# Kernel optimization log

Hardware: AMD Instinct MI355X
Metric: run time of the kernel (lower is better)

The kernel has to match this reference:

```python
import jax, jax.numpy as jnp
import numpy as np

N, E, F, H, C, B = 50000, 1_600_000, 128, 128, 10, 512


def setup_inputs() -> dict:
    key = jax.random.key(0)
    ks = jax.random.split(key, 12)
    inp = {
        "x": jax.random.normal(ks[0], (N, F), dtype=jnp.float32),
        "edge_index": jax.random.randint(ks[1], (2, E), 0, N, dtype=jnp.int32),
        "batch": jnp.sort(jax.random.randint(ks[2], (N,), 0, B, dtype=jnp.int32)),
        "edge_weight": jax.random.uniform(ks[3], (E,), dtype=jnp.float32),
        "W1": jax.random.normal(ks[4], (F, H), dtype=jnp.float32) * 0.05,
        "b1": jnp.zeros((H,), dtype=jnp.float32),
        "W2": jax.random.normal(ks[5], (H, H), dtype=jnp.float32) * 0.05,
        "b2": jnp.zeros((H,), dtype=jnp.float32),
        "W3": jax.random.normal(ks[6], (H, H), dtype=jnp.float32) * 0.05,
        "b3": jnp.zeros((H,), dtype=jnp.float32),
        "Wlin": jax.random.normal(ks[7], (H, C), dtype=jnp.float32) * 0.05,
        "blin": jnp.zeros((C,), dtype=jnp.float32),
    }
    return inp


def reference(x, edge_index, batch, edge_weight, W1, b1, W2, b2, W3, b3, Wlin, blin):
    n = x.shape[0]
    src, dst = edge_index[0], edge_index[1]
    loops = jnp.arange(n, dtype=src.dtype)
    src_f = jnp.concatenate([src, loops])  # edges + self-loops
    dst_f = jnp.concatenate([dst, loops])

    def make_norm(fill_value):
        # GCN symmetric normalization: D^-1/2 (A + fill*I) D^-1/2 on edge weights
        ew = jnp.concatenate([edge_weight, jnp.full((n,), fill_value, dtype=edge_weight.dtype)])
        deg = jax.ops.segment_sum(ew, dst_f, num_segments=n)
        dinv = jnp.where(deg > 0, deg ** -0.5, 0.0)
        return dinv[src_f] * ew * dinv[dst_f]

    # conv1 was built as GCNConv(in, hidden, out_channels) -> third positional arg is
    # `improved`, truthy => self-loop fill value 2.0; conv2/3 use 1.0.
    norm1 = make_norm(2.0)
    norm = make_norm(1.0)

    def gcn_conv(h, W, b, nrm):
        h = h @ W                                   # [N, H]
        msg = h[src_f] * nrm[:, None]               # [E+N, H] gather
        return jax.ops.segment_sum(msg, dst_f, num_segments=n) + b

    h = jax.nn.relu(gcn_conv(x, W1, b1, norm1))
    h = jax.nn.relu(gcn_conv(h, W2, b2, norm))
    h = gcn_conv(h, W3, b3, norm)

    # global_mean_pool over graph ids
    sums = jax.ops.segment_sum(h, batch, num_segments=B)
    cnt = jax.ops.segment_sum(jnp.ones((n,), dtype=h.dtype), batch, num_segments=B)
    pooled = sums / jnp.maximum(cnt, 1.0)[:, None]

    # dropout is identity in eval mode
    return pooled @ Wlin + blin
```

## Files before the change

kernel.cpp:

```cpp
#include <hip/hip_runtime.h>
#include <hip/hip_fp16.h>

#define F 128
#define HID 128
#define NCLS 10
#define CAP 80
#define NBIN 256
#define NPB 196
#define SCAP 7168
#define EPT 8
#define HLS 136

typedef short short8 __attribute__((ext_vector_type(8)));
typedef float float4v __attribute__((ext_vector_type(4)));
typedef float float2v __attribute__((ext_vector_type(2)));

__device__ __forceinline__ unsigned short f2bf(float f) {
    unsigned int u = __float_as_uint(f);
    unsigned int r = (u + 0x7FFFu + ((u >> 16) & 1u)) >> 16;
    return (unsigned short)r;
}
__device__ __forceinline__ float bf2f(unsigned int h) {
    return __uint_as_float(h << 16);
}
__device__ __forceinline__ unsigned char f2fp8(float a) {
    return (unsigned char)(__builtin_amdgcn_cvt_pk_fp8_f32(a, 0.f, 0, false) & 0xFF);
}

__global__ __launch_bounds__(256) void bin_prep_kernel(
    const int* __restrict__ ei, const float* __restrict__ ew,
    int* __restrict__ gcur, uint2* __restrict__ staging, int E, int nbb,
    const float* __restrict__ W1, const float* __restrict__ W2,
    const float* __restrict__ W3, const float* __restrict__ Wlin,
    const float* __restrict__ blin, const float* __restrict__ b3,
    unsigned short* __restrict__ Wp, unsigned short* __restrict__ Wp3s,
    float* __restrict__ bL) {
    __shared__ int lhist[NBIN];
    __shared__ int lscan[NBIN];
    __shared__ int lbase[NBIN];
    __shared__ uint2 lent[256 * EPT];
    int tid = threadIdx.x;

    if ((int)blockIdx.x < nbb) {
        lhist[tid] = 0;
        __syncthreads();

        unsigned int rpk[EPT];
        unsigned short rd[EPT];
        unsigned short rloc[EPT];
        int base = blockIdx.x * (256 * EPT);
#pragma unroll
        for (int i = 0; i < EPT; i++) {
            int e = base + tid + i * 256;
            if (e < E) {
                int s = ei[e];
                int d = ei[E + e];
                unsigned int q = (unsigned int)(ew[e] * 65535.0f + 0.5f);
                rpk[i] = (q << 16) | (unsigned int)s;
                rd[i] = (unsigned short)d;
                rloc[i] = (unsigned short)atomicAdd(&lhist[d / NPB], 1);
            } else {
                rpk[i] = 0u; rd[i] = 0; rloc[i] = 0xFFFF;
            }
        }
        __syncthreads();

        lscan[tid] = lhist[tid];
        __syncthreads();
        for (int off = 1; off < NBIN; off <<= 1) {
            int t = (tid >= off) ? lscan[tid - off] : 0;
            __syncthreads();
            lscan[tid] += t;
            __syncthreads();
        }
        lbase[tid] = atomicAdd(&gcur[tid], lhist[tid]);
        __syncthreads();

#pragma unroll
        for (int i = 0; i < EPT; i++) {
            if (rloc[i] != 0xFFFF) {
                int bin = (int)rd[i] / NPB;
                int slot = (lscan[bin] - lhist[bin]) + (int)rloc[i];
                lent[slot] = make_uint2(rpk[i], (unsigned int)rd[i]);
            }
        }
        __syncthreads();

        int total = lscan[NBIN - 1];
        for (int j = tid; j < total; j += 256) {
            uint2 t = lent[j];
            int bin = (int)t.y / NPB;
            int pos = lbase[bin] + (j - (lscan[bin] - lhist[bin]));
            if (pos < SCAP) staging[(size_t)bin * SCAP + pos] = t;
        }
    } else {
        int b = blockIdx.x - nbb;
        if (b < 128) {
            int widx = b >> 6;
            const float* W = (widx == 0) ? W1 : W2;
            int idx = (b & 63) * 256 + tid;
            int j = idx & 7;
            int l = (idx >> 3) & 63;
            int nt = (idx >> 9) & 7;
            int kt = idx >> 12;
            int k = kt * 32 + ((l >> 4) << 3) + j;
            int n = nt * 16 + (l & 15);
            Wp[widx * 16384 + idx] = f2bf(W[k * HID + n]);
        } else if (b < 136) {
            int idx = (b - 128) * 256 + tid;
            int j = idx & 7;
            int l = (idx >> 3) & 63;
            int kt = idx >> 9;
            int k = kt * 32 + ((l >> 4) << 3) + j;
            int n = l & 15;
            float v = 0.f;
            if (n < NCLS) {
                for (int m = 0; m < HID; m++)
                    v += W3[k * HID + m] * Wlin[m * NCLS + n];
            }
            Wp3s[idx] = f2bf(v);
        } else {
            if (tid < NCLS) {
                float bl = blin[tid];
                for (int j = 0; j < HID; j++) bl += b3[j] * Wlin[j * NCLS + tid];
                bL[tid] = bl;
            }
        }
    }
}

__global__ __launch_bounds__(1024, 8) void build_gemm1_kernel(
    const uint2* __restrict__ staging, const int* __restrict__ gcur,
    unsigned int* __restrict__ colw, int* __restrict__ cnt,
    float* __restrict__ dinv1, float* __restrict__ dinv0, int N, int nbins,
    const float* __restrict__ X, const unsigned short* __restrict__ Wp,
    unsigned char* __restrict__ Yb8) {
    __shared__ unsigned int lbuck[NPB * CAP];
    __shared__ int lcnt[NPB];
    int tid = threadIdx.x;

    if ((int)blockIdx.x < nbins) {
        int bin = blockIdx.x;
        int node0 = bin * NPB;

        for (int n = tid; n < NPB; n += 1024) lcnt[n] = 0;
        __syncthreads();

        int bcnt = gcur[bin];
        if (bcnt > SCAP) bcnt = SCAP;
        const uint2* st = staging + (size_t)bin * SCAP;
        for (int i = tid; i < bcnt; i += 1024) {
            uint2 t = st[i];
            int dl = (int)t.y - node0;
            int pos = atomicAdd(&lcnt[dl], 1);
            if (pos < CAP) lbuck[dl * CAP + pos] = t.x;
        }
        __syncthreads();

        for (int it = 0; it < NPB; it += 128) {
            int nl = it + (tid >> 3);
            int lane = tid & 7;
            if (nl < NPB) {
                int gn = node0 + nl;
                if (gn < N) {
                    int c = lcnt[nl];
                    if (c > CAP) c = CAP;
                    float s = 0.f;
                    for (int j = lane; j < c; j += 8)
                        s += (float)(lbuck[nl * CAP + j] >> 16);
                    s += __shfl_down(s, 4, 8);
                    s += __shfl_down(s, 2, 8);
                    s += __shfl_down(s, 1, 8);
                    if (lane == 0) {
                        float deg = s * (1.0f / 65535.0f);
                        cnt[gn] = c;
                        dinv1[gn] = 1.0f / sqrtf(deg + 2.0f);
                        dinv0[gn] = 1.0f / sqrtf(deg + 1.0f);
                    }
                }
            }
        }
        __syncthreads();

        int nvalid = N - node0;
        if (nvalid > NPB) nvalid = NPB;
        if (nvalid <= 0) return;
        int nslots = nvalid * (CAP / 4);
        uint4* dst4 = (uint4*)(colw + (size_t)node0 * CAP);
        const uint4* src4 = (const uint4*)lbuck;
        for (int i = tid; i < nslots; i += 1024) {
            int rowi = i / (CAP / 4);
            int slot = i - rowi * (CAP / 4);
            int c = lcnt[rowi];
            if (c > CAP) c = CAP;
            if (slot * 4 < c) dst4[i] = src4[i];
        }
    } else {
        int tile = blockIdx.x - nbins;
        int wave = tid >> 6, lane = tid & 63;
        int quad = lane >> 4, m = lane & 15;
        int row0 = tile * 256 + wave * 16;
        if (row0 >= N) return;
        int row = row0 + m;
        int rowc = row < N ? row : N - 1;

        short8 a[4];
        const float4* xrow = (const float4*)(X + (size_t)rowc * F);
#pragma unroll
        for (int kt = 0; kt < 4; kt++) {
            float4 p0 = xrow[kt * 8 + quad * 2];
            float4 p1 = xrow[kt * 8 + quad * 2 + 1];
            short8 v;
            v[0] = (short)f2bf(p0.x); v[1] = (short)f2bf(p0.y);
            v[2] = (short)f2bf(p0.z); v[3] = (short)f2bf(p0.w);
            v[4] = (short)f2bf(p1.x); v[5] = (short)f2bf(p1.y);
            v[6] = (short)f2bf(p1.z); v[7] = (short)f2bf(p1.w);
            a[kt] = v;
        }

#pragma unroll
        for (int nt = 0; nt < 8; nt++) {
            float4v c = {0.f, 0.f, 0.f, 0.f};
#pragma unroll
            for (int kt = 0; kt < 4; kt++) {
                short8 b = *(const short8*)(Wp + (((kt * 8 + nt) * 64 + lane) << 3));
                c = __builtin_amdgcn_mfma_f32_16x16x32_bf16(a[kt], b, c, 0, 0, 0);
            }
#pragma unroll
            for (int r = 0; r < 4; r++) {
                int gr = row0 + quad * 4 + r;
                if (gr < N) Yb8[(size_t)gr * HID + nt * 16 + m] = f2fp8(c[r]);
            }
        }
    }
}

__device__ __forceinline__ void agg_acc8(float f, const uint4& h,
                                         float2v acc[8]) {
    float2v fv = {f, f};
    acc[0] += fv * __builtin_amdgcn_cvt_pk_f32_fp8(h.x, false);
    acc[1] += fv * __builtin_amdgcn_cvt_pk_f32_fp8(h.x, true);
    acc[2] += fv * __builtin_amdgcn_cvt_pk_f32_fp8(h.y, false);
    acc[3] += fv * __builtin_amdgcn_cvt_pk_f32_fp8(h.y, true);
    acc[4] += fv * __builtin_amdgcn_cvt_pk_f32_fp8(h.z, false);
    acc[5] += fv * __builtin_amdgcn_cvt_pk_f32_fp8(h.z, true);
    acc[6] += fv * __builtin_amdgcn_cvt_pk_f32_fp8(h.w, false);
    acc[7] += fv * __builtin_amdgcn_cvt_pk_f32_fp8(h.w, true);
}

__device__ __forceinline__ void agg_b4(const unsigned int w[8], int t0, int fl,
                                       const uint4* __restrict__ hin4,
                                       const float* __restrict__ dinv,
                                       float2v acc[8]) {
    uint4 h[4];
    float dv[4];
#pragma unroll
    for (int t = 0; t < 4; t++) h[t] = hin4[(w[t0 + t] & 0xFFFFu) * 8 + fl];
#pragma unroll
    for (int t = 0; t < 4; t++) dv[t] = dinv[w[t0 + t] & 0xFFFFu];
#pragma unroll
    for (int t = 0; t < 4; t++) {
        float f = (float)(w[t0 + t] >> 16) * (1.0f / 65535.0f) * dv[t];
        agg_acc8(f, h[t], acc);
    }
}

__device__ __forceinline__ void agg_p32(unsigned int pk, int q, int fl,
                                        const uint4* __restrict__ hin4,
                                        const float* __restrict__ dinv,
                                        float2v acc[8]) {
    unsigned int w[8];
#pragma unroll
    for (int t = 0; t < 4; t++) {
        w[2 * t]     = (unsigned int)__shfl((int)pk, t * 8 + 2 * q, 32);
        w[2 * t + 1] = (unsigned int)__shfl((int)pk, t * 8 + 2 * q + 1, 32);
    }
    agg_b4(w, 0, fl, hin4, dinv, acc);
    agg_b4(w, 4, fl, hin4, dinv, acc);
}

__device__ __forceinline__ void agg_p8(unsigned int pk, int j0, int q, int fl,
                                       const uint4* __restrict__ hin4,
                                       const float* __restrict__ dinv,
                                       float2v acc[8]) {
    unsigned int w0 = (unsigned int)__shfl((int)pk, j0 + 2 * q, 32);
    unsigned int w1 = (unsigned int)__shfl((int)pk, j0 + 2 * q + 1, 32);
    uint4 h0 = hin4[(w0 & 0xFFFFu) * 8 + fl];
    uint4 h1 = hin4[(w1 & 0xFFFFu) * 8 + fl];
    float d0 = dinv[w0 & 0xFFFFu];
    float d1 = dinv[w1 & 0xFFFFu];
    agg_acc8((float)(w0 >> 16) * (1.0f / 65535.0f) * d0, h0, acc);
    agg_acc8((float)(w1 >> 16) * (1.0f / 65535.0f) * d1, h1, acc);
}

__device__ __forceinline__ void agg_node_fp8(int g, int lane,
                                             const unsigned char* __restrict__ hin,
                                             const unsigned int* __restrict__ colw,
                                             const int* __restrict__ cnt,
                                             const float* __restrict__ dinv,
                                             float fill,
                                             const float* __restrict__ bias,
                                             unsigned short* __restrict__ hl_row) {
    float dv = dinv[g];
    int c = cnt[g];
    if (c > CAP) c = CAP;
    const unsigned int* row = colw + (size_t)g * CAP;
    const uint4* hin4 = (const uint4*)hin;

    unsigned int pk[3];
#pragma unroll
    for (int k = 0; k < 3; k++) {
        int idx = lane + k * 32;
        pk[k] = (idx < c) ? row[idx] : 0u;
    }

    int q = lane >> 3;
    int fl = lane & 7;

    float2v acc[8];
#pragma unroll
    for (int i = 0; i < 8; i++) acc[i] = (float2v){0.f, 0.f};

    agg_p32(pk[0], q, fl, hin4, dinv, acc);
    if (c > 32) {
        int cc = c - 32;
        if (cc > 32) cc = 32;
        for (int j = 0; j < cc; j += 8) agg_p8(pk[1], j, q, fl, hin4, dinv, acc);
    }
    if (c > 64) {
        int cc = c - 64;
        for (int j = 0; j < cc; j += 8) agg_p8(pk[2], j, q, fl, hin4, dinv, acc);
    }

#pragma unroll
    for (int i = 0; i < 8; i++) {
        acc[i][0] += __shfl_down(acc[i][0], 16, 32);
        acc[i][1] += __shfl_down(acc[i][1], 16, 32);
        acc[i][0] += __shfl_down(acc[i][0], 8, 32);
        acc[i][1] += __shfl_down(acc[i][1], 8, 32);
    }

    if (q == 0) {
        uint4 hv = hin4[(size_t)g * 8 + fl];
        float2v ws = {fill * dv, fill * dv};
        float2v dvv = {dv, dv};
        acc[0] = (acc[0] + ws * __builtin_amdgcn_cvt_pk_f32_fp8(hv.x, false)) * dvv;
        acc[1] = (acc[1] + ws * __builtin_amdgcn_cvt_pk_f32_fp8(hv.x, true)) * dvv;
        acc[2] = (acc[2] + ws * __builtin_amdgcn_cvt_pk_f32_fp8(hv.y, false)) * dvv;
        acc[3] = (acc[3] + ws * __builtin_amdgcn_cvt_pk_f32_fp8(hv.y, true)) * dvv;
        acc[4] = (acc[4] + ws * __builtin_amdgcn_cvt_pk_f32_fp8(hv.z, false)) * dvv;
        acc[5] = (acc[5] + ws * __builtin_amdgcn_cvt_pk_f32_fp8(hv.z, true)) * dvv;
        acc[6] = (acc[6] + ws * __builtin_amdgcn_cvt_pk_f32_fp8(hv.w, false)) * dvv;
        acc[7] = (acc[7] + ws * __builtin_amdgcn_cvt_pk_f32_fp8(hv.w, true)) * dvv;

        const float2v* b2 = (const float2v*)(bias + fl * 16);
        uint4 o0, o1;
        unsigned int ow[8];
#pragma unroll
        for (int i = 0; i < 8; i++) {
            float2v v = acc[i] + b2[i];
            float v0 = fmaxf(v[0], 0.f);
            float v1 = fmaxf(v[1], 0.f);
            ow[i] = (unsigned int)f2bf(v0) | ((unsigned int)f2bf(v1) << 16);
        }
        o0 = make_uint4(ow[0], ow[1], ow[2], ow[3]);
        o1 = make_uint4(ow[4], ow[5], ow[6], ow[7]);
        *(uint4*)(hl_row + fl * 16) = o0;
        *(uint4*)(hl_row + fl * 16 + 8) = o1;
    }
}

__global__ __launch_bounds__(512) void agg_gemm128_kernel(const unsigned char* __restrict__ hin,
                                                          const unsigned int* __restrict__ colw,
                                                          const int* __restrict__ cnt,
                                                          const float* __restrict__ dinv,
                                                          const float* __restrict__ bias,
                                                          const unsigned short* __restrict__ Wp2,
                                                          unsigned char* __restrict__ Yb8,
                                                          int N) {
    __shared__ unsigned short hl[16 * HLS];
    __shared__ unsigned char Ol8[16 * 128];

    int tid = threadIdx.x;
    int gl = tid >> 5, lane = tid & 31;
    int row0 = blockIdx.x * 16;
    int g = row0 + gl;

    if (g < N) {
        agg_node_fp8(g, lane, hin, colw, cnt, dinv, 2.0f, bias, hl + gl * HLS);
    } else if ((lane >> 3) == 0) {
        *(uint4*)(hl + gl * HLS + (lane & 7) * 16) = make_uint4(0u, 0u, 0u, 0u);
        *(uint4*)(hl + gl * HLS + (lane & 7) * 16 + 8) = make_uint4(0u, 0u, 0u, 0u);
    }
    __syncthreads();

    int nt = tid >> 6;
    int lane64 = tid & 63;
    int quad = lane64 >> 4, m = lane64 & 15;

    short8 a[4];
#pragma unroll
    for (int kt = 0; kt < 4; kt++)
        a[kt] = *(const short8*)(hl + m * HLS + kt * 32 + quad * 8);

    float4v c = {0.f, 0.f, 0.f, 0.f};
#pragma unroll
    for (int kt = 0; kt < 4; kt++) {
        short8 b = *(const short8*)(Wp2 + (((kt * 8 + nt) * 64 + lane64) << 3));
        c = __builtin_amdgcn_mfma_f32_16x16x32_bf16(a[kt], b, c, 0, 0, 0);
    }
#pragma unroll
    for (int r = 0; r < 4; r++)
        Ol8[(quad * 4 + r) * 128 + nt * 16 + m] = f2fp8(c[r]);
    __syncthreads();

    if (tid < 128) {
        int gr = row0 + (tid >> 3);
        if (gr < N)
            ((uint4*)(Yb8 + (size_t)gr * 128))[tid & 7] = ((const uint4*)Ol8)[tid];
    }
}

__global__ __launch_bounds__(512) void agg_gemm16_kernel(const unsigned char* __restrict__ hin,
                                                         const unsigned int* __restrict__ colw,
                                                         const int* __restrict__ cnt,
                                                         const float* __restrict__ dinv,
                                                         const float* __restrict__ bias,
                                                         const unsigned short* __restrict__ Wp3s,
                                                         unsigned short* __restrict__ g3s,
                                                         int N) {
    __shared__ unsigned short hl[16 * HLS];

    int tid = threadIdx.x;
    int gl = tid >> 5, lane = tid & 31;
    int row0 = blockIdx.x * 16;
    int g = row0 + gl;

    if (g < N) {
        agg_node_fp8(g, lane, hin, colw, cnt, dinv, 1.0f, bias, hl + gl * HLS);
    } else if ((lane >> 3) == 0) {
        *(uint4*)(hl + gl * HLS + (lane & 7) * 16) = make_uint4(0u, 0u, 0u, 0u);
        *(uint4*)(hl + gl * HLS + (lane & 7) * 16 + 8) = make_uint4(0u, 0u, 0u, 0u);
    }
    __syncthreads();

    if (tid < 64) {
        int lane64 = tid;
        int quad = lane64 >> 4, m = lane64 & 15;
        short8 a[4];
#pragma unroll
        for (int kt = 0; kt < 4; kt++)
            a[kt] = *(const short8*)(hl + m * HLS + kt * 32 + quad * 8);
        float4v c = {0.f, 0.f, 0.f, 0.f};
#pragma unroll
        for (int kt = 0; kt < 4; kt++) {
            short8 b = *(const short8*)(Wp3s + ((kt * 64 + lane64) << 3));
            c = __builtin_amdgcn_mfma_f32_16x16x32_bf16(a[kt], b, c, 0, 0, 0);
        }
#pragma unroll
        for (int r = 0; r < 4; r++) {
            int gr = row0 + quad * 4 + r;
            if (gr < N) g3s[(size_t)gr * 16 + m] = f2bf(c[r]);
        }
    }
}

__device__ __forceinline__ void agg3_slot(unsigned int pk, int lane2off,
                                          const unsigned short* __restrict__ g3s,
                                          const float* __restrict__ dinv,
                                          float& ax, float& ay) {
    unsigned int w[8];
    unsigned int h[8];
    float dvv[8];
#pragma unroll
    for (int t = 0; t < 8; t++)
        w[t] = (unsigned int)__shfl((int)pk, t, 8);
#pragma unroll
    for (int t = 0; t < 8; t++)
        h[t] = *(const unsigned int*)(g3s + (w[t] & 0xFFFFu) * 16 + lane2off);
#pragma unroll
    for (int t = 0; t < 8; t++)
        dvv[t] = dinv[w[t] & 0xFFFFu];
#pragma unroll
    for (int t = 0; t < 8; t++) {
        float f = (float)(w[t] >> 16) * (1.0f / 65535.0f) * dvv[t];
        ax += f * bf2f(h[t] & 0xFFFFu);
        ay += f * bf2f(h[t] >> 16);
    }
}

__global__ __launch_bounds__(256) void agg3_kernel(const unsigned short* __restrict__ g3s,
                                                   const unsigned int* __restrict__ colw,
                                                   const int* __restrict__ cnt,
                                                   const float* __restrict__ dinv,
                                                   unsigned short* __restrict__ h3s, int N) {
    int g = (blockIdx.x * blockDim.x + threadIdx.x) >> 3;
    int lane = threadIdx.x & 7;
    if (g >= N) return;

    float dv = dinv[g];
    int c = cnt[g];
    if (c > CAP) c = CAP;
    const unsigned int* row = colw + (size_t)g * CAP;
    int lane2off = lane * 2;

    unsigned int pk[10];
#pragma unroll
    for (int k = 0; k < 10; k++) {
        int idx = lane + k * 8;
        pk[k] = (idx < c) ? row[idx] : 0u;
    }

    float ax = 0.f, ay = 0.f;
#pragma unroll
    for (int slot = 0; slot < 10; slot++) {
        int base = slot * 8;
        if (c > base) agg3_slot(pk[slot], lane2off, g3s, dinv, ax, ay);
    }

    unsigned int hv = *(const unsigned int*)(g3s + (size_t)g * 16 + lane2off);
    ax = (ax + dv * bf2f(hv & 0xFFFFu)) * dv;
    ay = (ay + dv * bf2f(hv >> 16)) * dv;

    unsigned int o = (unsigned int)f2bf(ax) | ((unsigned int)f2bf(ay) << 16);
    *(unsigned int*)(h3s + (size_t)g * 16 + lane2off) = o;
}

__global__ __launch_bounds__(256) void pool3_kernel(const unsigned short* __restrict__ h3s,
                                                    const int* __restrict__ batch,
                                                    const float* __restrict__ bL,
                                                    const float* __restrict__ blin,
                                                    float* __restrict__ out, int N, int B) {
    int wave = (blockIdx.x * blockDim.x + threadIdx.x) >> 6;
    int lane = threadIdx.x & 63;
    if (wave >= B) return;
    int g = wave;
    int d = lane & 15, sub = lane >> 4;

    int lo = 0, hi = N;
    while (lo < hi) { int m = (lo + hi) >> 1; if (batch[m] < g) lo = m + 1; else hi = m; }
    int s0 = lo;
    hi = N;
    while (lo < hi) { int m = (lo + hi) >> 1; if (batch[m] < g + 1) lo = m + 1; else hi = m; }
    int s1 = lo;

    float p = 0.f;
    for (int v = s0 + sub; v < s1; v += 4)
        p += bf2f((unsigned int)h3s[(size_t)v * 16 + d]);
    p += __shfl_down(p, 32, 64);
    p += __shfl_down(p, 16, 64);

    if (lane < NCLS) {
        int cntv = s1 - s0;
        float r = (cntv > 0) ? (p / (float)cntv + bL[d]) : blin[d];
        out[g * NCLS + d] = r;
    }
}

extern "C" void kernel_launch(void* const* d_in, const int* in_sizes, int n_in,
                              void* d_out, int out_size, void* d_ws, size_t ws_size,
                              hipStream_t stream) {
    const float* x    = (const float*)d_in[0];
    const int*   ei   = (const int*)d_in[1];
    const int*   batch= (const int*)d_in[2];
    const float* ew   = (const float*)d_in[3];
    const float* W1   = (const float*)d_in[4];
    const float* b1   = (const float*)d_in[5];
    const float* W2   = (const float*)d_in[6];
    const float* b2   = (const float*)d_in[7];
    const float* W3   = (const float*)d_in[8];
    const float* b3   = (const float*)d_in[9];
    const float* Wlin = (const float*)d_in[10];
    const float* blin = (const float*)d_in[11];
    float* out = (float*)d_out;

    int N = in_sizes[0] / F;
    int E = in_sizes[1] / 2;
    int B = out_size / NCLS;

    char* p = (char*)d_ws;
    auto alloc = [&](size_t bytes) -> void* {
        void* r = (void*)p;
        p += (bytes + 255) & ~(size_t)255;
        return r;
    };
    int*            cnt   = (int*)alloc((size_t)N * 4);
    float*          dinv1 = (float*)alloc((size_t)N * 4);
    float*          dinv0 = (float*)alloc((size_t)N * 4);
    int*            gcur  = (int*)alloc(NBIN * 4);
    float*          bL    = (float*)alloc(16 * 4);
    unsigned int*   colw  = (unsigned int*)alloc((size_t)N * CAP * 4);
    unsigned short* Wp    = (unsigned short*)alloc(2 * 16384 * 2);
    unsigned short* Wp3s  = (unsigned short*)alloc(2048 * 2);
    unsigned char*  bufA  = (unsigned char*)alloc((size_t)N * HID);
    unsigned char*  bufB  = (unsigned char*)alloc((size_t)N * HID);
    unsigned short* g3s   = (unsigned short*)alloc((size_t)N * 16 * 2);
    unsigned short* h3s   = (unsigned short*)alloc((size_t)N * 16 * 2);
    uint2*          staging = (uint2*)alloc((size_t)NBIN * SCAP * 8);

    int tb = 256;
    int nbins = (N + NPB - 1) / NPB;
    int nbb = (E + tb * EPT - 1) / (tb * EPT);
    int g1tiles = (N + 255) / 256;

    hipMemsetAsync(gcur, 0, NBIN * 4, stream);
    bin_prep_kernel<<<nbb + 137, tb, 0, stream>>>(ei, ew, gcur, staging, E, nbb,
                                                  W1, W2, W3, Wlin, blin, b3,
                                                  Wp, Wp3s, bL);
    build_gemm1_kernel<<<nbins + g1tiles, 1024, 0, stream>>>(staging, gcur, colw, cnt,
                                                             dinv1, dinv0, N, nbins,
                                                             x, Wp, bufA);

    int fused_blocks = (N + 15) / 16;
    int agg3_blocks = ((N * 8) + tb - 1) / tb;

    agg_gemm128_kernel<<<fused_blocks, 512, 0, stream>>>(bufA, colw, cnt, dinv1, b1,
                                                         Wp + 16384, bufB, N);
    agg_gemm16_kernel<<<fused_blocks, 512, 0, stream>>>(bufB, colw, cnt, dinv0, b2,
                                                        Wp3s, g3s, N);
    agg3_kernel<<<agg3_blocks, tb, 0, stream>>>(g3s, colw, cnt, dinv0, h3s, N);
    pool3_kernel<<<((B * 64) + tb - 1) / tb, tb, 0, stream>>>(h3s, batch, bL, blin,
                                                              out, N, B);
}
```

Baseline: 231.9 us.

## Fuse tail aggregation layers and pooling into one cooperative persistent kernel

Replaces the four tail launches (layer-2 agg+GEMM, layer-3 agg+GEMM, final aggregation, mean pool) with one cooperative kernel that loops over tiles and separates the phases with grid-wide syncs. It also folds the source-side dinv factor into the stored features (scaling GEMM outputs by dinv0), so the later gathers skip the per-edge dinv loads. This removes launch gaps and tail drain between the kernels. In exchange it adds grid barriers, caps the grid at 1024 persistent blocks with forced occupancy of 8 blocks of 512 threads, and changes fp8/bf16 rounding because values are pre-scaled before quantization.

```diff
diff --git a/kernel.cpp b/kernel.cpp
--- a/kernel.cpp
+++ b/kernel.cpp
@@ -1,5 +1,8 @@
 #include <hip/hip_runtime.h>
 #include <hip/hip_fp16.h>
+#include <hip/hip_cooperative_groups.h>
+
+namespace cg = cooperative_groups;
 
 #define F 128
 #define HID 128
@@ -248,6 +251,7 @@
     acc[7] += fv * __builtin_amdgcn_cvt_pk_f32_fp8(h.w, true);
 }
 
+template <bool GD>
 __device__ __forceinline__ void agg_b4(const unsigned int w[8], int t0, int fl,
                                        const uint4* __restrict__ hin4,
                                        const float* __restrict__ dinv,
@@ -256,15 +260,19 @@
     float dv[4];
 #pragma unroll
     for (int t = 0; t < 4; t++) h[t] = hin4[(w[t0 + t] & 0xFFFFu) * 8 + fl];
-#pragma unroll
-    for (int t = 0; t < 4; t++) dv[t] = dinv[w[t0 + t] & 0xFFFFu];
+    if (GD) {
+#pragma unroll
+        for (int t = 0; t < 4; t++) dv[t] = dinv[w[t0 + t] & 0xFFFFu];
+    }
 #pragma unroll
     for (int t = 0; t < 4; t++) {
-        float f = (float)(w[t0 + t] >> 16) * (1.0f / 65535.0f) * dv[t];
+        float f = (float)(w[t0 + t] >> 16) * (1.0f / 65535.0f);
+        if (GD) f *= dv[t];
         agg_acc8(f, h[t], acc);
     }
 }
 
+template <bool GD>
 __device__ __forceinline__ void agg_p32(unsigned int pk, int q, int fl,
                                         const uint4* __restrict__ hin4,
                                         const float* __restrict__ dinv,
@@ -275,10 +283,11 @@
         w[2 * t]     = (unsigned int)__shfl((int)pk, t * 8 + 2 * q, 32);
         w[2 * t + 1] = (unsigned int)__shfl((int)pk, t * 8 + 2 * q + 1, 32);
     }
-    agg_b4(w, 0, fl, hin4, dinv, acc);
-    agg_b4(w, 4, fl, hin4, dinv, acc);
-}
-
+    agg_b4<GD>(w, 0, fl, hin4, dinv, acc);
+    agg_b4<GD>(w, 4, fl, hin4, dinv, acc);
+}
+
+template <bool GD>
 __device__ __forceinline__ void agg_p8(unsigned int pk, int j0, int q, int fl,
                                        const uint4* __restrict__ hin4,
                                        const float* __restrict__ dinv,
@@ -287,12 +296,14 @@
     unsigned int w1 = (unsigned int)__shfl((int)pk, j0 + 2 * q + 1, 32);
     uint4 h0 = hin4[(w0 & 0xFFFFu) * 8 + fl];
     uint4 h1 = hin4[(w1 & 0xFFFFu) * 8 + fl];
-    float d0 = dinv[w0 & 0xFFFFu];
-    float d1 = dinv[w1 & 0xFFFFu];
-    agg_acc8((float)(w0 >> 16) * (1.0f / 65535.0f) * d0, h0, acc);
-    agg_acc8((float)(w1 >> 16) * (1.0f / 65535.0f) * d1, h1, acc);
-}
-
+    float f0 = (float)(w0 >> 16) * (1.0f / 65535.0f);
+    float f1 = (float)(w1 >> 16) * (1.0f / 65535.0f);
+    if (GD) { f0 *= dinv[w0 & 0xFFFFu]; f1 *= dinv[w1 & 0xFFFFu]; }
+    agg_acc8(f0, h0, acc);
+    agg_acc8(f1, h1, acc);
+}
+
+template <bool GD>
 __device__ __forceinline__ void agg_node_fp8(int g, int lane,
                                              const unsigned char* __restrict__ hin,
                                              const unsigned int* __restrict__ colw,
@@ -321,15 +332,15 @@
 #pragma unroll
     for (int i = 0; i < 8; i++) acc[i] = (float2v){0.f, 0.f};
 
-    agg_p32(pk[0], q, fl, hin4, dinv, acc);
+    agg_p32<GD>(pk[0], q, fl, hin4, dinv, acc);
     if (c > 32) {
         int cc = c - 32;
         if (cc > 32) cc = 32;
-        for (int j = 0; j < cc; j += 8) agg_p8(pk[1], j, q, fl, hin4, dinv, acc);
+        for (int j = 0; j < cc; j += 8) agg_p8<GD>(pk[1], j, q, fl, hin4, dinv, acc);
     }
     if (c > 64) {
         int cc = c - 64;
-        for (int j = 0; j < cc; j += 8) agg_p8(pk[2], j, q, fl, hin4, dinv, acc);
+        for (int j = 0; j < cc; j += 8) agg_p8<GD>(pk[2], j, q, fl, hin4, dinv, acc);
     }
 
 #pragma unroll
@@ -342,7 +353,8 @@
 
     if (q == 0) {
         uint4 hv = hin4[(size_t)g * 8 + fl];
-        float2v ws = {fill * dv, fill * dv};
+        float wsv = GD ? fill * dv : fill;
+        float2v ws = {wsv, wsv};
         float2v dvv = {dv, dv};
         acc[0] = (acc[0] + ws * __builtin_amdgcn_cvt_pk_f32_fp8(hv.x, false)) * dvv;
         acc[1] = (acc[1] + ws * __builtin_amdgcn_cvt_pk_f32_fp8(hv.x, true)) * dvv;
@@ -370,190 +382,175 @@
     }
 }
 
-__global__ __launch_bounds__(512) void agg_gemm128_kernel(const unsigned char* __restrict__ hin,
-                                                          const unsigned int* __restrict__ colw,
-                                                          const int* __restrict__ cnt,
-                                                          const float* __restrict__ dinv,
-                                                          const float* __restrict__ bias,
-                                                          const unsigned short* __restrict__ Wp2,
-                                                          unsigned char* __restrict__ Yb8,
-                                                          int N) {
+__global__ __launch_bounds__(512, 8) void fused_tail_kernel(
+    const unsigned char* __restrict__ bufA,
+    const unsigned int* __restrict__ colw, const int* __restrict__ cnt,
+    const float* __restrict__ dinv1, const float* __restrict__ dinv0,
+    const float* __restrict__ b1, const float* __restrict__ b2,
+    const unsigned short* __restrict__ Wp2,
+    const unsigned short* __restrict__ Wp3s,
+    unsigned char* __restrict__ bufB, unsigned short* __restrict__ g3s,
+    unsigned short* __restrict__ h3s,
+    const int* __restrict__ batch, const float* __restrict__ bL,
+    const float* __restrict__ blin, float* __restrict__ out,
+    int N, int B) {
+    cg::grid_group grid = cg::this_grid();
     __shared__ unsigned short hl[16 * HLS];
     __shared__ unsigned char Ol8[16 * 128];
 
     int tid = threadIdx.x;
     int gl = tid >> 5, lane = tid & 31;
-    int row0 = blockIdx.x * 16;
-    int g = row0 + gl;
-
-    if (g < N) {
-        agg_node_fp8(g, lane, hin, colw, cnt, dinv, 2.0f, bias, hl + gl * HLS);
-    } else if ((lane >> 3) == 0) {
-        *(uint4*)(hl + gl * HLS + (lane & 7) * 16) = make_uint4(0u, 0u, 0u, 0u);
-        *(uint4*)(hl + gl * HLS + (lane & 7) * 16 + 8) = make_uint4(0u, 0u, 0u, 0u);
-    }
-    __syncthreads();
-
-    int nt = tid >> 6;
-    int lane64 = tid & 63;
-    int quad = lane64 >> 4, m = lane64 & 15;
-
-    short8 a[4];
-#pragma unroll
-    for (int kt = 0; kt < 4; kt++)
-        a[kt] = *(const short8*)(hl + m * HLS + kt * 32 + quad * 8);
-
-    float4v c = {0.f, 0.f, 0.f, 0.f};
-#pragma unroll
-    for (int kt = 0; kt < 4; kt++) {
-        short8 b = *(const short8*)(Wp2 + (((kt * 8 + nt) * 64 + lane64) << 3));
-        c = __builtin_amdgcn_mfma_f32_16x16x32_bf16(a[kt], b, c, 0, 0, 0);
-    }
-#pragma unroll
-    for (int r = 0; r < 4; r++)
-        Ol8[(quad * 4 + r) * 128 + nt * 16 + m] = f2fp8(c[r]);
-    __syncthreads();
-
-    if (tid < 128) {
-        int gr = row0 + (tid >> 3);
-        if (gr < N)
-            ((uint4*)(Yb8 + (size_t)gr * 128))[tid & 7] = ((const uint4*)Ol8)[tid];
-    }
-}
-
-__global__ __launch_bounds__(512) void agg_gemm16_kernel(const unsigned char* __restrict__ hin,
-                                                         const unsigned int* __restrict__ colw,
-                                                         const int* __restrict__ cnt,
-                                                         const float* __restrict__ dinv,
-                                                         const float* __restrict__ bias,
-                                                         const unsigned short* __restrict__ Wp3s,
-                                                         unsigned short* __restrict__ g3s,
-                                                         int N) {
-    __shared__ unsigned short hl[16 * HLS];
-
-    int tid = threadIdx.x;
-    int gl = tid >> 5, lane = tid & 31;
-    int row0 = blockIdx.x * 16;
-    int g = row0 + gl;
-
-    if (g < N) {
-        agg_node_fp8(g, lane, hin, colw, cnt, dinv, 1.0f, bias, hl + gl * HLS);
-    } else if ((lane >> 3) == 0) {
-        *(uint4*)(hl + gl * HLS + (lane & 7) * 16) = make_uint4(0u, 0u, 0u, 0u);
-        *(uint4*)(hl + gl * HLS + (lane & 7) * 16 + 8) = make_uint4(0u, 0u, 0u, 0u);
-    }
-    __syncthreads();
-
-    if (tid < 64) {
-        int lane64 = tid;
+    int ntiles = (N + 15) >> 4;
+
+    for (int t = blockIdx.x; t < ntiles; t += gridDim.x) {
+        int row0 = t * 16;
+        int g = row0 + gl;
+        if (g < N) {
+            agg_node_fp8<true>(g, lane, bufA, colw, cnt, dinv1, 2.0f, b1,
+                               hl + gl * HLS);
+        } else if ((lane >> 3) == 0) {
+            *(uint4*)(hl + gl * HLS + (lane & 7) * 16) = make_uint4(0u, 0u, 0u, 0u);
+            *(uint4*)(hl + gl * HLS + (lane & 7) * 16 + 8) = make_uint4(0u, 0u, 0u, 0u);
+        }
+        __syncthreads();
+
+        int nt = tid >> 6;
+        int lane64 = tid & 63;
         int quad = lane64 >> 4, m = lane64 & 15;
+
         short8 a[4];
 #pragma unroll
         for (int kt = 0; kt < 4; kt++)
             a[kt] = *(const short8*)(hl + m * HLS + kt * 32 + quad * 8);
+
         float4v c = {0.f, 0.f, 0.f, 0.f};
 #pragma unroll
         for (int kt = 0; kt < 4; kt++) {
-            short8 b = *(const short8*)(Wp3s + ((kt * 64 + lane64) << 3));
+            short8 b = *(const short8*)(Wp2 + (((kt * 8 + nt) * 64 + lane64) << 3));
             c = __builtin_amdgcn_mfma_f32_16x16x32_bf16(a[kt], b, c, 0, 0, 0);
         }
 #pragma unroll
         for (int r = 0; r < 4; r++) {
             int gr = row0 + quad * 4 + r;
-            if (gr < N) g3s[(size_t)gr * 16 + m] = f2bf(c[r]);
-        }
-    }
-}
-
-__device__ __forceinline__ void agg3_slot(unsigned int pk, int lane2off,
-                                          const unsigned short* __restrict__ g3s,
-                                          const float* __restrict__ dinv,
-                                          float& ax, float& ay) {
-    unsigned int w[8];
-    unsigned int h[8];
-    float dvv[8];
-#pragma unroll
-    for (int t = 0; t < 8; t++)
-        w[t] = (unsigned int)__shfl((int)pk, t, 8);
-#pragma unroll
-    for (int t = 0; t < 8; t++)
-        h[t] = *(const unsigned int*)(g3s + (w[t] & 0xFFFFu) * 16 + lane2off);
-#pragma unroll
-    for (int t = 0; t < 8; t++)
-        dvv[t] = dinv[w[t] & 0xFFFFu];
-#pragma unroll
-    for (int t = 0; t < 8; t++) {
-        float f = (float)(w[t] >> 16) * (1.0f / 65535.0f) * dvv[t];
-        ax += f * bf2f(h[t] & 0xFFFFu);
-        ay += f * bf2f(h[t] >> 16);
-    }
-}
-
-__global__ __launch_bounds__(256) void agg3_kernel(const unsigned short* __restrict__ g3s,
-                                                   const unsigned int* __restrict__ colw,
-                                                   const int* __restrict__ cnt,
-                                                   const float* __restrict__ dinv,
-                                                   unsigned short* __restrict__ h3s, int N) {
-    int g = (blockIdx.x * blockDim.x + threadIdx.x) >> 3;
-    int lane = threadIdx.x & 7;
-    if (g >= N) return;
-
-    float dv = dinv[g];
-    int c = cnt[g];
-    if (c > CAP) c = CAP;
-    const unsigned int* row = colw + (size_t)g * CAP;
-    int lane2off = lane * 2;
-
-    unsigned int pk[10];
-#pragma unroll
-    for (int k = 0; k < 10; k++) {
-        int idx = lane + k * 8;
-        pk[k] = (idx < c) ? row[idx] : 0u;
-    }
-
-    float ax = 0.f, ay = 0.f;
-#pragma unroll
-    for (int slot = 0; slot < 10; slot++) {
-        int base = slot * 8;
-        if (c > base) agg3_slot(pk[slot], lane2off, g3s, dinv, ax, ay);
-    }
-
-    unsigned int hv = *(const unsigned int*)(g3s + (size_t)g * 16 + lane2off);
-    ax = (ax + dv * bf2f(hv & 0xFFFFu)) * dv;
-    ay = (ay + dv * bf2f(hv >> 16)) * dv;
-
-    unsigned int o = (unsigned int)f2bf(ax) | ((unsigned int)f2bf(ay) << 16);
-    *(unsigned int*)(h3s + (size_t)g * 16 + lane2off) = o;
-}
-
-__global__ __launch_bounds__(256) void pool3_kernel(const unsigned short* __restrict__ h3s,
-                                                    const int* __restrict__ batch,
-                                                    const float* __restrict__ bL,
-                                                    const float* __restrict__ blin,
-                                                    float* __restrict__ out, int N, int B) {
-    int wave = (blockIdx.x * blockDim.x + threadIdx.x) >> 6;
-    int lane = threadIdx.x & 63;
-    if (wave >= B) return;
-    int g = wave;
-    int d = lane & 15, sub = lane >> 4;
-
-    int lo = 0, hi = N;
-    while (lo < hi) { int m = (lo + hi) >> 1; if (batch[m] < g) lo = m + 1; else hi = m; }
-    int s0 = lo;
-    hi = N;
-    while (lo < hi) { int m = (lo + hi) >> 1; if (batch[m] < g + 1) lo = m + 1; else hi = m; }
-    int s1 = lo;
-
-    float p = 0.f;
-    for (int v = s0 + sub; v < s1; v += 4)
-        p += bf2f((unsigned int)h3s[(size_t)v * 16 + d]);
-    p += __shfl_down(p, 32, 64);
-    p += __shfl_down(p, 16, 64);
-
-    if (lane < NCLS) {
-        int cntv = s1 - s0;
-        float r = (cntv > 0) ? (p / (float)cntv + bL[d]) : blin[d];
-        out[g * NCLS + d] = r;
+            float sc = (gr < N) ? dinv0[gr] : 0.f;
+            Ol8[(quad * 4 + r) * 128 + nt * 16 + m] = f2fp8(c[r] * sc);
+        }
+        __syncthreads();
+
+        if (tid < 128) {
+            int gr = row0 + (tid >> 3);
+            if (gr < N)
+                ((uint4*)(bufB + (size_t)gr * 128))[tid & 7] = ((const uint4*)Ol8)[tid];
+        }
+    }
+    grid.sync();
+
+    for (int t = blockIdx.x; t < ntiles; t += gridDim.x) {
+        int row0 = t * 16;
+        int g = row0 + gl;
+        if (g < N) {
+            agg_node_fp8<false>(g, lane, bufB, colw, cnt, dinv0, 1.0f, b2,
+                                hl + gl * HLS);
+        } else if ((lane >> 3) == 0) {
+            *(uint4*)(hl + gl * HLS + (lane & 7) * 16) = make_uint4(0u, 0u, 0u, 0u);
+            *(uint4*)(hl + gl * HLS + (lane & 7) * 16 + 8) = make_uint4(0u, 0u, 0u, 0u);
+        }
+        __syncthreads();
+
+        if (tid < 64) {
+            int lane64 = tid;
+            int quad = lane64 >> 4, m = lane64 & 15;
+            short8 a[4];
+#pragma unroll
+            for (int kt = 0; kt < 4; kt++)
+                a[kt] = *(const short8*)(hl + m * HLS + kt * 32 + quad * 8);
+            float4v c = {0.f, 0.f, 0.f, 0.f};
+#pragma unroll
+            for (int kt = 0; kt < 4; kt++) {
+                short8 b = *(const short8*)(Wp3s + ((kt * 64 + lane64) << 3));
+                c = __builtin_amdgcn_mfma_f32_16x16x32_bf16(a[kt], b, c, 0, 0, 0);
+            }
+#pragma unroll
+            for (int r = 0; r < 4; r++) {
+                int gr = row0 + quad * 4 + r;
+                if (gr < N)
+                    g3s[(size_t)gr * 16 + m] = f2bf(c[r] * dinv0[gr]);
+            }
+        }
+        __syncthreads();
+    }
+    grid.sync();
+
+    {
+        int lane8 = tid & 7;
+        int lane2off = lane8 * 2;
+        for (int g = blockIdx.x * 64 + (tid >> 3); g < N; g += gridDim.x * 64) {
+            float dv = dinv0[g];
+            int c = cnt[g];
+            if (c > CAP) c = CAP;
+            const unsigned int* row = colw + (size_t)g * CAP;
+
+            unsigned int pk[10];
+#pragma unroll
+            for (int k = 0; k < 10; k++) {
+                int idx = lane8 + k * 8;
+                pk[k] = (idx < c) ? row[idx] : 0u;
+            }
+
+            float ax = 0.f, ay = 0.f;
+#pragma unroll
+            for (int slot = 0; slot < 10; slot++) {
+                if (c > slot * 8) {
+                    unsigned int w[8];
+                    unsigned int h[8];
+#pragma unroll
+                    for (int tt = 0; tt < 8; tt++)
+                        w[tt] = (unsigned int)__shfl((int)pk[slot], tt, 8);
+#pragma unroll
+                    for (int tt = 0; tt < 8; tt++)
+                        h[tt] = *(const unsigned int*)(g3s + (w[tt] & 0xFFFFu) * 16 + lane2off);
+#pragma unroll
+                    for (int tt = 0; tt < 8; tt++) {
+                        float f = (float)(w[tt] >> 16) * (1.0f / 65535.0f);
+                        ax += f * bf2f(h[tt] & 0xFFFFu);
+                        ay += f * bf2f(h[tt] >> 16);
+                    }
+                }
+            }
+
+            unsigned int hv = *(const unsigned int*)(g3s + (size_t)g * 16 + lane2off);
+            ax = (ax + bf2f(hv & 0xFFFFu)) * dv;
+            ay = (ay + bf2f(hv >> 16)) * dv;
+
+            unsigned int o = (unsigned int)f2bf(ax) | ((unsigned int)f2bf(ay) << 16);
+            *(unsigned int*)(h3s + (size_t)g * 16 + lane2off) = o;
+        }
+    }
+    grid.sync();
+
+    {
+        int lane64 = tid & 63;
+        int d = lane64 & 15, sub = lane64 >> 4;
+        for (int g = blockIdx.x * 8 + (tid >> 6); g < B; g += gridDim.x * 8) {
+            int lo = 0, hi = N;
+            while (lo < hi) { int m = (lo + hi) >> 1; if (batch[m] < g) lo = m + 1; else hi = m; }
+            int s0 = lo;
+            hi = N;
+            while (lo < hi) { int m = (lo + hi) >> 1; if (batch[m] < g + 1) lo = m + 1; else hi = m; }
+            int s1 = lo;
+
+            float p = 0.f;
+            for (int v = s0 + sub; v < s1; v += 4)
+                p += bf2f((unsigned int)h3s[(size_t)v * 16 + d]);
+            p += __shfl_down(p, 32, 64);
+            p += __shfl_down(p, 16, 64);
+
+            if (lane64 < NCLS) {
+                int cntv = s1 - s0;
+                float r = (cntv > 0) ? (p / (float)cntv + bL[d]) : blin[d];
+                out[g * NCLS + d] = r;
+            }
+        }
     }
 }
 
@@ -611,14 +608,24 @@
                                                              dinv1, dinv0, N, nbins,
                                                              x, Wp, bufA);
 
-    int fused_blocks = (N + 15) / 16;
-    int agg3_blocks = ((N * 8) + tb - 1) / tb;
-
-    agg_gemm128_kernel<<<fused_blocks, 512, 0, stream>>>(bufA, colw, cnt, dinv1, b1,
-                                                         Wp + 16384, bufB, N);
-    agg_gemm16_kernel<<<fused_blocks, 512, 0, stream>>>(bufB, colw, cnt, dinv0, b2,
-                                                        Wp3s, g3s, N);
-    agg3_kernel<<<agg3_blocks, tb, 0, stream>>>(g3s, colw, cnt, dinv0, h3s, N);
-    pool3_kernel<<<((B * 64) + tb - 1) / tb, tb, 0, stream>>>(h3s, batch, bL, blin,
-                                                              out, N, B);
-}
+    static int coop_grid = -1;
+    if (coop_grid < 0) {
+        int maxb = 0, ncu = 0;
+        hipOccupancyMaxActiveBlocksPerMultiprocessor(&maxb, fused_tail_kernel, 512, 0);
+        hipDeviceGetAttribute(&ncu, hipDeviceAttributeMultiprocessorCount, 0);
+        if (maxb < 1) maxb = 1;
+        if (ncu < 1) ncu = 256;
+        long g = (long)maxb * ncu;
+        coop_grid = (g > 1024) ? 1024 : (int)g;
+    }
+
+    const unsigned short* Wp2 = Wp + 16384;
+    void* kargs[] = {
+        (void*)&bufA, (void*)&colw, (void*)&cnt, (void*)&dinv1, (void*)&dinv0,
+        (void*)&b1, (void*)&b2, (void*)&Wp2, (void*)&Wp3s,
+        (void*)&bufB, (void*)&g3s, (void*)&h3s,
+        (void*)&batch, (void*)&bL, (void*)&blin, (void*)&out,
+        (void*)&N, (void*)&B};
+    hipLaunchCooperativeKernel((void*)fused_tail_kernel, dim3(coop_grid),
+                               dim3(512), kargs, 0, stream);
+}
```

Result: slower. 541.3 us (+133.4%).
